# Optimization experiments

Hardware: AMD Instinct MI355X
Metric: run time of the kernel (lower is better)

Reference implementation:

```python
import jax, jax.numpy as jnp
import numpy as np

E = 16        # n_routed_experts
K = 2         # n_activated_experts (top-k)
DIM = 1024    # model dim
INTER = 704   # moe_inter_dim
B, S = 4, 1024


def setup_inputs() -> dict:
    key = jax.random.key(0)
    ks = jax.random.split(key, 5)
    x = jax.random.normal(ks[0], (B, S, DIM), dtype=jnp.float32)
    Wg = jax.random.normal(ks[1], (E, DIM), dtype=jnp.float32) * 0.02   # gate (Linear, no bias)
    W1 = jax.random.normal(ks[2], (E, DIM, INTER), dtype=jnp.float32) * 0.02
    W3 = jax.random.normal(ks[3], (E, DIM, INTER), dtype=jnp.float32) * 0.02
    W2 = jax.random.normal(ks[4], (E, INTER, DIM), dtype=jnp.float32) * 0.02
    return {"x": x, "Wg": Wg, "W1": W1, "W2": W2, "W3": W3}


def reference(x, Wg, W1, W2, W3):
    # Single-process semantics of MoEWithAll2All: the all2all dispatch/combine is
    # pure communication; the math is: softmax router -> top-k -> renormalize ->
    # per-expert SwiGLU MLP on routed tokens -> weighted combine at original slots.
    Bb, Ss, D = x.shape
    xf = x.reshape(-1, D)                              # [N, D], N = B*S
    logits = xf @ Wg.T                                 # [N, E]
    probs = jax.nn.softmax(logits, axis=-1)
    topw, topi = jax.lax.top_k(probs, K)               # [N, K]
    topw = topw / topw.sum(axis=-1, keepdims=True)
    # gates[n, e] = routed weight of token n for expert e (0 if not routed):
    # identical math to the masked gather/scatter dispatch in the original.
    gates = (jax.nn.one_hot(topi, E, dtype=xf.dtype) * topw[..., None]).sum(axis=1)  # [N, E]
    out = jnp.zeros_like(xf)
    for e in range(E):                                 # small fixed loop over experts
        h = jax.nn.silu(xf @ W1[e]) * (xf @ W3[e])     # SwiGLU expert, [N, INTER]
        out = out + gates[:, e:e + 1] * (h @ W2[e])    # combine with gate weights
    return out.reshape(Bb, Ss, D)
```

## Files before the change

### kernel.cpp

```cpp
#include <hip/hip_runtime.h>

#define NTOK 4096
#define DDIM 1024
#define IDIM 704
#define NEXP 16
#define NSLOT 8192
#define MAXT 128
#define NPAD1 768

typedef __attribute__((ext_vector_type(8))) short bf16x8;
typedef __attribute__((ext_vector_type(4))) float f32x4;
typedef __attribute__((ext_vector_type(4))) unsigned short us4;
typedef __attribute__((ext_vector_type(8))) unsigned short us8;

__device__ __forceinline__ unsigned short f2bf(float f) {
  union { float f; unsigned int u; } v; v.f = f;
  unsigned int r = v.u + 0x7fffu + ((v.u >> 16) & 1u);
  return (unsigned short)(r >> 16);
}

__device__ __forceinline__ void gload_lds16(const void* g, void* l) {
  __builtin_amdgcn_global_load_lds((const __attribute__((address_space(1))) void*)g,
                                   (__attribute__((address_space(3))) void*)l, 16, 0, 0);
}

__global__ void k_convert(const float* __restrict__ x, unsigned short* __restrict__ Xb) {
  int i = blockIdx.x * 256 + threadIdx.x;
  f32x4 v = ((const f32x4*)x)[i];
  us4 o;
#pragma unroll
  for (int j = 0; j < 4; ++j) o[j] = f2bf(v[j]);
  ((us4*)Xb)[i] = o;
}

__global__ void k_wtrans(const float* __restrict__ src, unsigned short* __restrict__ dst,
                         int ksz, int nsz) {
  int e = blockIdx.z;
  int k0 = blockIdx.x * 64, n0 = blockIdx.y * 64;
  int npad = gridDim.y * 64;
  src += (size_t)e * ksz * nsz;
  dst += (size_t)e * npad * ksz;
  int t = threadIdx.x;
  int nr = t >> 3, kc0 = (t & 7) * 8;
  if (n0 >= nsz) {
    us8 z = (us8)0;
#pragma unroll
    for (int p = 0; p < 2; ++p)
      *(us8*)(dst + (size_t)(n0 + nr + p * 32) * ksz + k0 + kc0) = z;
    return;
  }
  __shared__ unsigned short lds[64 * 76];
  int nc = (t & 15) * 4, kr = t >> 4;
#pragma unroll
  for (int p = 0; p < 4; ++p) {
    f32x4 v = *(const f32x4*)(src + (size_t)(k0 + kr + p * 16) * nsz + n0 + nc);
    us4 o;
#pragma unroll
    for (int j = 0; j < 4; ++j) o[j] = f2bf(v[j]);
    *(us4*)(lds + (kr + p * 16) * 76 + nc) = o;
  }
  __syncthreads();
#pragma unroll
  for (int p = 0; p < 2; ++p) {
    int row = nr + p * 32;
    us8 o;
#pragma unroll
    for (int j = 0; j < 8; ++j) o[j] = lds[(kc0 + j) * 76 + row];
    *(us8*)(dst + (size_t)(n0 + row) * ksz + k0 + kc0) = o;
  }
}

__global__ void k_router(const float* __restrict__ x, const float* __restrict__ Wg,
                         int* __restrict__ tok_e, float* __restrict__ tok_w) {
  int lane = threadIdx.x & 63;
  int wv = threadIdx.x >> 6;
  int t = blockIdx.x * 4 + wv;
  const f32x4* xr = (const f32x4*)(x + (size_t)t * DDIM);
  f32x4 xv[4];
#pragma unroll
  for (int c = 0; c < 4; ++c) xv[c] = xr[c * 64 + lane];
  float p[NEXP];
#pragma unroll
  for (int e = 0; e < NEXP; ++e) {
    const f32x4* wr = (const f32x4*)(Wg + (size_t)e * DDIM);
    float s = 0.f;
#pragma unroll
    for (int c = 0; c < 4; ++c) {
      f32x4 w4 = wr[c * 64 + lane];
      s += xv[c][0]*w4[0] + xv[c][1]*w4[1] + xv[c][2]*w4[2] + xv[c][3]*w4[3];
    }
    p[e] = s;
  }
#pragma unroll
  for (int off = 32; off >= 1; off >>= 1) {
#pragma unroll
    for (int e = 0; e < NEXP; ++e) p[e] += __shfl_xor(p[e], off);
  }
  int i0 = 0; float b0 = p[0];
#pragma unroll
  for (int e = 1; e < NEXP; ++e) if (p[e] > b0) { b0 = p[e]; i0 = e; }
  int i1 = -1; float b1 = -3.4e38f;
#pragma unroll
  for (int e = 0; e < NEXP; ++e) if (e != i0 && p[e] > b1) { b1 = p[e]; i1 = e; }
  if (lane == 0) {
    float w0 = 1.f / (1.f + __expf(b1 - b0));
    tok_e[2*t] = i0; tok_e[2*t+1] = i1;
    tok_w[2*t] = w0; tok_w[2*t+1] = 1.f - w0;
  }
}

__global__ void k_count_scan(const int* __restrict__ tok_e, int* __restrict__ counts,
                             int* __restrict__ offsets, int* __restrict__ ntiles,
                             int* __restrict__ tile_e, int* __restrict__ tile_m0) {
  __shared__ int h[256 * 17];
  __shared__ int counts_s[NEXP];
  int t = threadIdx.x;
  int c[NEXP];
#pragma unroll
  for (int e = 0; e < NEXP; ++e) c[e] = 0;
  for (int i = t; i < NSLOT; i += 256) {
    int te = tok_e[i];
#pragma unroll
    for (int e = 0; e < NEXP; ++e) c[e] += (te == e) ? 1 : 0;
  }
#pragma unroll
  for (int e = 0; e < NEXP; ++e) h[t * 17 + e] = c[e];
  __syncthreads();
  if (t < NEXP) {
    int s = 0;
    for (int i = 0; i < 256; ++i) s += h[i * 17 + t];
    counts_s[t] = s;
    counts[t] = s;
  }
  __syncthreads();
  if (t == 0) {
    int acc = 0, nt = 0;
    for (int e = 0; e < NEXP; ++e) {
      offsets[e] = acc;
      int cc = counts_s[e];
      for (int m0 = 0; m0 < cc; m0 += 128) { tile_e[nt] = e; tile_m0[nt] = m0; ++nt; }
      acc += cc;
    }
    offsets[NEXP] = acc;
    *ntiles = nt;
  }
}

__global__ void k_scatter2(const int* __restrict__ tok_e, const float* __restrict__ tok_w,
                           const int* __restrict__ offsets, int* __restrict__ token_map,
                           float* __restrict__ gate_w, int* __restrict__ slot_of) {
  int e = blockIdx.x;
  int t = threadIdx.x, lane = t & 63, wv = t >> 6;
  int te[32]; float tw[32];
#pragma unroll
  for (int c = 0; c < 32; ++c) {
    te[c] = tok_e[c * 256 + t];
    tw[c] = tok_w[c * 256 + t];
  }
  __shared__ int wsum[4];
  int run = offsets[e];
  unsigned long long below = (lane == 63) ? 0x7fffffffffffffffull : ((1ull << lane) - 1ull);
#pragma unroll 1
  for (int c = 0; c < 32; ++c) {
    bool f = (te[c] == e);
    unsigned long long m = __ballot(f);
    if (lane == 0) wsum[wv] = __popcll(m);
    __syncthreads();
    int base = run;
    for (int w = 0; w < wv; ++w) base += wsum[w];
    int tot = wsum[0] + wsum[1] + wsum[2] + wsum[3];
    if (f) {
      int i = c * 256 + t;
      int slot = base + __popcll(m & below);
      token_map[slot] = i >> 1;
      gate_w[slot] = tw[c];
      slot_of[i] = slot;
    }
    run += tot;
    __syncthreads();
  }
}

__global__ __launch_bounds__(256, 2)
void k_gemm1(const unsigned short* __restrict__ Xb, const unsigned short* __restrict__ W1T,
             const unsigned short* __restrict__ W3T, const int* __restrict__ token_map,
             const float* __restrict__ gate_w, const int* __restrict__ ntiles,
             const int* __restrict__ tile_e, const int* __restrict__ tile_m0,
             const int* __restrict__ offsets, const int* __restrict__ counts,
             unsigned short* __restrict__ H) {
  int ty = blockIdx.y;
  if (ty >= *ntiles) return;
  int e = tile_e[ty], m0 = tile_m0[ty];
  int n0 = blockIdx.x * 128;
  int base_slot = offsets[e] + m0;
  int cnt = counts[e] - m0; if (cnt > 128) cnt = 128;

  __shared__ unsigned short As[128 * 32];
  __shared__ unsigned short B1s[128 * 32];
  __shared__ unsigned short B3s[128 * 32];

  int t = threadIdx.x;
  int row = t >> 2, kc = (t & 3) * 8;
  int r0i = base_slot + row;      if (r0i > NSLOT - 1) r0i = NSLOT - 1;
  int r1i = base_slot + 64 + row; if (r1i > NSLOT - 1) r1i = NSLOT - 1;
  const unsigned short* ag0 = Xb + (size_t)token_map[r0i] * DDIM + kc;
  const unsigned short* ag1 = Xb + (size_t)token_map[r1i] * DDIM + kc;
  const unsigned short* b1g0 = W1T + ((size_t)e * NPAD1 + n0 + row) * DDIM + kc;
  const unsigned short* b1g1 = b1g0 + (size_t)64 * DDIM;
  const unsigned short* b3g0 = W3T + ((size_t)e * NPAD1 + n0 + row) * DDIM + kc;
  const unsigned short* b3g1 = b3g0 + (size_t)64 * DDIM;
  unsigned short* asd0 = As + t * 8;   unsigned short* asd1 = As + 2048 + t * 8;
  unsigned short* b1d0 = B1s + t * 8;  unsigned short* b1d1 = B1s + 2048 + t * 8;
  unsigned short* b3d0 = B3s + t * 8;  unsigned short* b3d1 = B3s + 2048 + t * 8;

  int lane = t & 63, wv = t >> 6;
  int wm = (wv >> 1) * 64, wn = (wv & 1) * 64;
  int lm = lane & 15, kg = lane >> 4;
  int ao[4], bo[4];
#pragma unroll
  for (int i = 0; i < 4; ++i) {
    ao[i] = (wm + i * 16 + lm) * 32 + kg * 8;
    bo[i] = (wn + i * 16 + lm) * 32 + kg * 8;
  }

  f32x4 acc1[4][4], acc3[4][4];
#pragma unroll
  for (int i = 0; i < 4; ++i)
#pragma unroll
    for (int j = 0; j < 4; ++j) { acc1[i][j] = 0.f; acc3[i][j] = 0.f; }

  for (int k0 = 0; k0 < DDIM; k0 += 32) {
    __syncthreads();
    gload_lds16(ag0 + k0, asd0);
    gload_lds16(ag1 + k0, asd1);
    gload_lds16(b1g0 + k0, b1d0);
    gload_lds16(b1g1 + k0, b1d1);
    gload_lds16(b3g0 + k0, b3d0);
    gload_lds16(b3g1 + k0, b3d1);
    __syncthreads();
    bf16x8 av[4], b1v[4], b3v[4];
#pragma unroll
    for (int i = 0; i < 4; ++i) {
      av[i]  = *(const bf16x8*)(As + ao[i]);
      b1v[i] = *(const bf16x8*)(B1s + bo[i]);
      b3v[i] = *(const bf16x8*)(B3s + bo[i]);
    }
#pragma unroll
    for (int mi = 0; mi < 4; ++mi)
#pragma unroll
      for (int ni = 0; ni < 4; ++ni) {
        acc1[mi][ni] = __builtin_amdgcn_mfma_f32_16x16x32_bf16(av[mi], b1v[ni], acc1[mi][ni], 0, 0, 0);
        acc3[mi][ni] = __builtin_amdgcn_mfma_f32_16x16x32_bf16(av[mi], b3v[ni], acc3[mi][ni], 0, 0, 0);
      }
  }

#pragma unroll
  for (int mi = 0; mi < 4; ++mi)
#pragma unroll
    for (int r = 0; r < 4; ++r) {
      int orow = wm + mi * 16 + kg * 4 + r;
      if (orow < cnt) {
        int slot = base_slot + orow;
        float gw = gate_w[slot];
        unsigned short* hrow = H + (size_t)slot * IDIM;
#pragma unroll
        for (int ni = 0; ni < 4; ++ni) {
          int nn = n0 + wn + ni * 16 + lm;
          if (nn < IDIM) {
            float v1 = acc1[mi][ni][r];
            float v3 = acc3[mi][ni][r];
            float h = v1 / (1.f + __expf(-v1)) * v3 * gw;
            hrow[nn] = f2bf(h);
          }
        }
      }
    }
}

__global__ __launch_bounds__(256, 3)
void k_gemm2(const unsigned short* __restrict__ H, const unsigned short* __restrict__ W2T,
             const int* __restrict__ ntiles, const int* __restrict__ tile_e,
             const int* __restrict__ tile_m0, const int* __restrict__ offsets,
             const int* __restrict__ counts, float* __restrict__ O2) {
  int ty = blockIdx.y;
  if (ty >= *ntiles) return;
  int e = tile_e[ty], m0 = tile_m0[ty];
  int n0 = blockIdx.x * 128;
  int base_slot = offsets[e] + m0;
  int cnt = counts[e] - m0; if (cnt > 128) cnt = 128;

  __shared__ unsigned short As[128 * 32];
  __shared__ unsigned short Bs[128 * 32];

  int t = threadIdx.x;
  int row = t >> 2, kc = (t & 3) * 8;
  int r0i = base_slot + row;      if (r0i > NSLOT - 1) r0i = NSLOT - 1;
  int r1i = base_slot + 64 + row; if (r1i > NSLOT - 1) r1i = NSLOT - 1;
  const unsigned short* ag0 = H + (size_t)r0i * IDIM + kc;
  const unsigned short* ag1 = H + (size_t)r1i * IDIM + kc;
  const unsigned short* bg0 = W2T + ((size_t)e * DDIM + n0 + row) * IDIM + kc;
  const unsigned short* bg1 = bg0 + (size_t)64 * IDIM;
  unsigned short* asd0 = As + t * 8;  unsigned short* asd1 = As + 2048 + t * 8;
  unsigned short* bd0 = Bs + t * 8;   unsigned short* bd1 = Bs + 2048 + t * 8;

  int lane = t & 63, wv = t >> 6;
  int wm = (wv >> 1) * 64, wn = (wv & 1) * 64;
  int lm = lane & 15, kg = lane >> 4;
  int ao[4], bo[4];
#pragma unroll
  for (int i = 0; i < 4; ++i) {
    ao[i] = (wm + i * 16 + lm) * 32 + kg * 8;
    bo[i] = (wn + i * 16 + lm) * 32 + kg * 8;
  }

  f32x4 acc[4][4];
#pragma unroll
  for (int i = 0; i < 4; ++i)
#pragma unroll
    for (int j = 0; j < 4; ++j) acc[i][j] = 0.f;

  for (int k0 = 0; k0 < IDIM; k0 += 32) {
    __syncthreads();
    gload_lds16(ag0 + k0, asd0);
    gload_lds16(ag1 + k0, asd1);
    gload_lds16(bg0 + k0, bd0);
    gload_lds16(bg1 + k0, bd1);
    __syncthreads();
    bf16x8 av[4], bv[4];
#pragma unroll
    for (int i = 0; i < 4; ++i) {
      av[i] = *(const bf16x8*)(As + ao[i]);
      bv[i] = *(const bf16x8*)(Bs + bo[i]);
    }
#pragma unroll
    for (int mi = 0; mi < 4; ++mi)
#pragma unroll
      for (int ni = 0; ni < 4; ++ni)
        acc[mi][ni] = __builtin_amdgcn_mfma_f32_16x16x32_bf16(av[mi], bv[ni], acc[mi][ni], 0, 0, 0);
  }

#pragma unroll
  for (int mi = 0; mi < 4; ++mi)
#pragma unroll
    for (int r = 0; r < 4; ++r) {
      int orow = wm + mi * 16 + kg * 4 + r;
      if (orow < cnt) {
        float* op = O2 + (size_t)(base_slot + orow) * DDIM + n0;
#pragma unroll
        for (int ni = 0; ni < 4; ++ni)
          op[wn + ni * 16 + lm] = acc[mi][ni][r];
      }
    }
}

__global__ void k_combine(const float* __restrict__ O2, const int* __restrict__ slot_of,
                          float* __restrict__ out) {
  int tk = blockIdx.x, tt = threadIdx.x;
  int s0 = slot_of[2 * tk], s1 = slot_of[2 * tk + 1];
  f32x4 a = ((const f32x4*)(O2 + (size_t)s0 * DDIM))[tt];
  f32x4 b = ((const f32x4*)(O2 + (size_t)s1 * DDIM))[tt];
  ((f32x4*)(out + (size_t)tk * DDIM))[tt] = a + b;
}

extern "C" void kernel_launch(void* const* d_in, const int* in_sizes, int n_in,
                              void* d_out, int out_size, void* d_ws, size_t ws_size,
                              hipStream_t stream) {
  const float* x  = (const float*)d_in[0];
  const float* Wg = (const float*)d_in[1];
  const float* W1 = (const float*)d_in[2];
  const float* W2 = (const float*)d_in[3];
  const float* W3 = (const float*)d_in[4];
  float* out = (float*)d_out;

  char* ws = (char*)d_ws;
  size_t off = 0;
  unsigned short* Xb = (unsigned short*)(ws + off); off += (size_t)NTOK * DDIM * 2;
  unsigned short* H  = (unsigned short*)(ws + off); off += (size_t)NSLOT * IDIM * 2;
  float* O2 = (float*)(ws + off); off += (size_t)NSLOT * DDIM * 4;
  unsigned short* W1T = (unsigned short*)(ws + off); off += (size_t)NEXP * NPAD1 * DDIM * 2;
  unsigned short* W3T = (unsigned short*)(ws + off); off += (size_t)NEXP * NPAD1 * DDIM * 2;
  unsigned short* W2T = (unsigned short*)(ws + off); off += (size_t)NEXP * DDIM * IDIM * 2;
  int* counts  = (int*)(ws + off); off += 64;
  int* offsets = (int*)(ws + off); off += 128;
  int* ntiles  = (int*)(ws + off); off += 64;
  int* tile_e  = (int*)(ws + off); off += MAXT * 4;
  int* tile_m0 = (int*)(ws + off); off += MAXT * 4;
  int* tok_e   = (int*)(ws + off); off += NSLOT * 4;
  float* tok_w = (float*)(ws + off); off += NSLOT * 4;
  int* token_map = (int*)(ws + off); off += NSLOT * 4;
  float* gate_w  = (float*)(ws + off); off += NSLOT * 4;
  int* slot_of   = (int*)(ws + off); off += NSLOT * 4;

  k_convert<<<4096, 256, 0, stream>>>(x, Xb);
  k_router<<<1024, 256, 0, stream>>>(x, Wg, tok_e, tok_w);
  k_count_scan<<<1, 256, 0, stream>>>(tok_e, counts, offsets, ntiles, tile_e, tile_m0);
  k_scatter2<<<NEXP, 256, 0, stream>>>(tok_e, tok_w, offsets, token_map, gate_w, slot_of);
  k_wtrans<<<dim3(16, 12, NEXP), 256, 0, stream>>>(W1, W1T, DDIM, IDIM);
  k_wtrans<<<dim3(16, 12, NEXP), 256, 0, stream>>>(W3, W3T, DDIM, IDIM);
  k_wtrans<<<dim3(11, 16, NEXP), 256, 0, stream>>>(W2, W2T, IDIM, DDIM);
  k_gemm1<<<dim3(6, 80), 256, 0, stream>>>(Xb, W1T, W3T, token_map, gate_w, ntiles, tile_e,
                                           tile_m0, offsets, counts, H);
  k_gemm2<<<dim3(8, 80), 256, 0, stream>>>(H, W2T, ntiles, tile_e, tile_m0, offsets, counts, O2);
  k_combine<<<4096, 256, 0, stream>>>(O2, slot_of, out);
}
```

Measured before the change: 317.7 us.

## Fuse bf16 convert into router, swizzle wtrans LDS, remap GEMM tiles per XCD

Folds the x-to-bf16 conversion into the router kernel, which already reads x, so one kernel launch and one full read of x go away. The weight-transpose kernel now loads four rows per thread into registers and writes them to an XOR-swizzled, unpadded LDS tile so the transposed reads can use 16-byte vector loads. Both GEMMs switch to a 1D grid that remaps blocks so that groups of blocks on the same XCD share expert tiles, aiming for better L2 reuse. The W2 transpose is moved after gemm1. The main risks are the tile remap logic and any change in LDS bank conflicts.

```diff
diff --git a/kernel.cpp b/kernel.cpp
--- a/kernel.cpp
+++ b/kernel.cpp
@@ -24,61 +24,23 @@
                                    (__attribute__((address_space(3))) void*)l, 16, 0, 0);
 }
 
-__global__ void k_convert(const float* __restrict__ x, unsigned short* __restrict__ Xb) {
-  int i = blockIdx.x * 256 + threadIdx.x;
-  f32x4 v = ((const f32x4*)x)[i];
-  us4 o;
-#pragma unroll
-  for (int j = 0; j < 4; ++j) o[j] = f2bf(v[j]);
-  ((us4*)Xb)[i] = o;
-}
-
-__global__ void k_wtrans(const float* __restrict__ src, unsigned short* __restrict__ dst,
-                         int ksz, int nsz) {
-  int e = blockIdx.z;
-  int k0 = blockIdx.x * 64, n0 = blockIdx.y * 64;
-  int npad = gridDim.y * 64;
-  src += (size_t)e * ksz * nsz;
-  dst += (size_t)e * npad * ksz;
-  int t = threadIdx.x;
-  int nr = t >> 3, kc0 = (t & 7) * 8;
-  if (n0 >= nsz) {
-    us8 z = (us8)0;
-#pragma unroll
-    for (int p = 0; p < 2; ++p)
-      *(us8*)(dst + (size_t)(n0 + nr + p * 32) * ksz + k0 + kc0) = z;
-    return;
-  }
-  __shared__ unsigned short lds[64 * 76];
-  int nc = (t & 15) * 4, kr = t >> 4;
-#pragma unroll
-  for (int p = 0; p < 4; ++p) {
-    f32x4 v = *(const f32x4*)(src + (size_t)(k0 + kr + p * 16) * nsz + n0 + nc);
-    us4 o;
-#pragma unroll
-    for (int j = 0; j < 4; ++j) o[j] = f2bf(v[j]);
-    *(us4*)(lds + (kr + p * 16) * 76 + nc) = o;
-  }
-  __syncthreads();
-#pragma unroll
-  for (int p = 0; p < 2; ++p) {
-    int row = nr + p * 32;
-    us8 o;
-#pragma unroll
-    for (int j = 0; j < 8; ++j) o[j] = lds[(kc0 + j) * 76 + row];
-    *(us8*)(dst + (size_t)(n0 + row) * ksz + k0 + kc0) = o;
-  }
-}
-
 __global__ void k_router(const float* __restrict__ x, const float* __restrict__ Wg,
-                         int* __restrict__ tok_e, float* __restrict__ tok_w) {
+                         int* __restrict__ tok_e, float* __restrict__ tok_w,
+                         unsigned short* __restrict__ Xb) {
   int lane = threadIdx.x & 63;
   int wv = threadIdx.x >> 6;
   int t = blockIdx.x * 4 + wv;
   const f32x4* xr = (const f32x4*)(x + (size_t)t * DDIM);
+  us4* xbr = (us4*)(Xb + (size_t)t * DDIM);
   f32x4 xv[4];
 #pragma unroll
-  for (int c = 0; c < 4; ++c) xv[c] = xr[c * 64 + lane];
+  for (int c = 0; c < 4; ++c) {
+    xv[c] = xr[c * 64 + lane];
+    us4 o;
+#pragma unroll
+    for (int j = 0; j < 4; ++j) o[j] = f2bf(xv[c][j]);
+    xbr[c * 64 + lane] = o;
+  }
   float p[NEXP];
 #pragma unroll
   for (int e = 0; e < NEXP; ++e) {
@@ -106,6 +68,47 @@
     float w0 = 1.f / (1.f + __expf(b1 - b0));
     tok_e[2*t] = i0; tok_e[2*t+1] = i1;
     tok_w[2*t] = w0; tok_w[2*t+1] = 1.f - w0;
+  }
+}
+
+__global__ void k_wtrans(const float* __restrict__ src, unsigned short* __restrict__ dst,
+                         int ksz, int nsz, int npad) {
+  int e = blockIdx.z;
+  int k0 = blockIdx.x * 64, n0 = blockIdx.y * 64;
+  src += (size_t)e * ksz * nsz;
+  dst += (size_t)e * npad * ksz;
+  int t = threadIdx.x;
+  if (n0 >= nsz) {
+    int nr = t >> 3, kc0 = (t & 7) * 8;
+    us8 z = (us8)(unsigned short)0;
+#pragma unroll
+    for (int p = 0; p < 2; ++p)
+      *(us8*)(dst + (size_t)(n0 + nr + p * 32) * ksz + k0 + kc0) = z;
+    return;
+  }
+  __shared__ unsigned short lds[64 * 64];
+  int kr4 = (t >> 4) * 4, nc4 = (t & 15) * 4;
+  f32x4 v[4];
+#pragma unroll
+  for (int j = 0; j < 4; ++j)
+    v[j] = *(const f32x4*)(src + (size_t)(k0 + kr4 + j) * nsz + n0 + nc4);
+  int c8 = kr4 >> 3, half = (kr4 >> 2) & 1;
+#pragma unroll
+  for (int i = 0; i < 4; ++i) {
+    us4 o;
+#pragma unroll
+    for (int j = 0; j < 4; ++j) o[j] = f2bf(v[j][i]);
+    int row = nc4 + i;
+    int addr = row * 64 + ((c8 ^ ((row >> 2) & 7)) << 3) + half * 4;
+    *(us4*)(lds + addr) = o;
+  }
+  __syncthreads();
+  int nr = t >> 3, kc8 = t & 7;
+#pragma unroll
+  for (int p = 0; p < 2; ++p) {
+    int row = nr + p * 32;
+    us8 o = *(const us8*)(lds + row * 64 + ((kc8 ^ ((row >> 2) & 7)) << 3));
+    *(us8*)(dst + (size_t)(n0 + row) * ksz + k0 + kc8 * 8) = o;
   }
 }
 
@@ -188,10 +191,14 @@
              const int* __restrict__ tile_e, const int* __restrict__ tile_m0,
              const int* __restrict__ offsets, const int* __restrict__ counts,
              unsigned short* __restrict__ H) {
-  int ty = blockIdx.y;
+  int idx = blockIdx.x;
+  int xcd = idx & 7, r = idx >> 3;
+  int g = (r >> 2) * 8 + xcd;
+  int mm = r & 3;
+  int ty = (g / 6) * 4 + mm;
   if (ty >= *ntiles) return;
+  int n0 = (g % 6) * 128;
   int e = tile_e[ty], m0 = tile_m0[ty];
-  int n0 = blockIdx.x * 128;
   int base_slot = offsets[e] + m0;
   int cnt = counts[e] - m0; if (cnt > 128) cnt = 128;
 
@@ -257,8 +264,8 @@
 #pragma unroll
   for (int mi = 0; mi < 4; ++mi)
 #pragma unroll
-    for (int r = 0; r < 4; ++r) {
-      int orow = wm + mi * 16 + kg * 4 + r;
+    for (int rr = 0; rr < 4; ++rr) {
+      int orow = wm + mi * 16 + kg * 4 + rr;
       if (orow < cnt) {
         int slot = base_slot + orow;
         float gw = gate_w[slot];
@@ -267,8 +274,8 @@
         for (int ni = 0; ni < 4; ++ni) {
           int nn = n0 + wn + ni * 16 + lm;
           if (nn < IDIM) {
-            float v1 = acc1[mi][ni][r];
-            float v3 = acc3[mi][ni][r];
+            float v1 = acc1[mi][ni][rr];
+            float v3 = acc3[mi][ni][rr];
             float h = v1 / (1.f + __expf(-v1)) * v3 * gw;
             hrow[nn] = f2bf(h);
           }
@@ -282,10 +289,14 @@
              const int* __restrict__ ntiles, const int* __restrict__ tile_e,
              const int* __restrict__ tile_m0, const int* __restrict__ offsets,
              const int* __restrict__ counts, float* __restrict__ O2) {
-  int ty = blockIdx.y;
+  int idx = blockIdx.x;
+  int xcd = idx & 7, r = idx >> 3;
+  int g = (r >> 2) * 8 + xcd;
+  int mm = r & 3;
+  int ty = (g >> 3) * 4 + mm;
   if (ty >= *ntiles) return;
+  int n0 = (g & 7) * 128;
   int e = tile_e[ty], m0 = tile_m0[ty];
-  int n0 = blockIdx.x * 128;
   int base_slot = offsets[e] + m0;
   int cnt = counts[e] - m0; if (cnt > 128) cnt = 128;
 
@@ -342,13 +353,13 @@
 #pragma unroll
   for (int mi = 0; mi < 4; ++mi)
 #pragma unroll
-    for (int r = 0; r < 4; ++r) {
-      int orow = wm + mi * 16 + kg * 4 + r;
+    for (int rr = 0; rr < 4; ++rr) {
+      int orow = wm + mi * 16 + kg * 4 + rr;
       if (orow < cnt) {
         float* op = O2 + (size_t)(base_slot + orow) * DDIM + n0;
 #pragma unroll
         for (int ni = 0; ni < 4; ++ni)
-          op[wn + ni * 16 + lm] = acc[mi][ni][r];
+          op[wn + ni * 16 + lm] = acc[mi][ni][rr];
       }
     }
 }
@@ -391,15 +402,14 @@
   float* gate_w  = (float*)(ws + off); off += NSLOT * 4;
   int* slot_of   = (int*)(ws + off); off += NSLOT * 4;
 
-  k_convert<<<4096, 256, 0, stream>>>(x, Xb);
-  k_router<<<1024, 256, 0, stream>>>(x, Wg, tok_e, tok_w);
+  k_router<<<1024, 256, 0, stream>>>(x, Wg, tok_e, tok_w, Xb);
   k_count_scan<<<1, 256, 0, stream>>>(tok_e, counts, offsets, ntiles, tile_e, tile_m0);
   k_scatter2<<<NEXP, 256, 0, stream>>>(tok_e, tok_w, offsets, token_map, gate_w, slot_of);
-  k_wtrans<<<dim3(16, 12, NEXP), 256, 0, stream>>>(W1, W1T, DDIM, IDIM);
-  k_wtrans<<<dim3(16, 12, NEXP), 256, 0, stream>>>(W3, W3T, DDIM, IDIM);
-  k_wtrans<<<dim3(11, 16, NEXP), 256, 0, stream>>>(W2, W2T, IDIM, DDIM);
-  k_gemm1<<<dim3(6, 80), 256, 0, stream>>>(Xb, W1T, W3T, token_map, gate_w, ntiles, tile_e,
-                                           tile_m0, offsets, counts, H);
-  k_gemm2<<<dim3(8, 80), 256, 0, stream>>>(H, W2T, ntiles, tile_e, tile_m0, offsets, counts, O2);
+  k_wtrans<<<dim3(16, 12, NEXP), 256, 0, stream>>>(W1, W1T, DDIM, IDIM, NPAD1);
+  k_wtrans<<<dim3(16, 12, NEXP), 256, 0, stream>>>(W3, W3T, DDIM, IDIM, NPAD1);
+  k_gemm1<<<480, 256, 0, stream>>>(Xb, W1T, W3T, token_map, gate_w, ntiles, tile_e,
+                                   tile_m0, offsets, counts, H);
+  k_wtrans<<<dim3(11, 16, NEXP), 256, 0, stream>>>(W2, W2T, IDIM, DDIM, DDIM);
+  k_gemm2<<<640, 256, 0, stream>>>(H, W2T, ntiles, tile_e, tile_m0, offsets, counts, O2);
   k_combine<<<4096, 256, 0, stream>>>(O2, slot_of, out);
 }
```

Result: faster. 308.1 us (-3.0%).
